# Optimization experiments

Measured on AMD Instinct MI355X. Metric: run time of the kernel, lower is better.

Reference implementation:

```python
import jax, jax.numpy as jnp
import numpy as np

K = 512
DIM = 256
BETA = 0.25


def setup_inputs() -> dict:
    key = jax.random.key(0)
    k1, k2 = jax.random.split(key)
    x = jax.random.normal(k1, (64, DIM, 32, 32), dtype=jnp.float32)
    lookup_table = jax.random.normal(k2, (K, DIM), dtype=jnp.float32)
    return {"x": x, "lookup_table": lookup_table}


def reference(x, lookup_table):
    b, d, h, w = x.shape
    # [b,d,h,w] -> [b*h*w, d]
    xf = jnp.transpose(x, (0, 2, 3, 1)).reshape(-1, d)
    # Squared Euclidean distances (argmin identical to torch.cdist argmin)
    d2 = (
        jnp.sum(xf * xf, axis=-1, keepdims=True)
        - 2.0 * (xf @ lookup_table.T)
        + jnp.sum(lookup_table * lookup_table, axis=-1)
    )  # [N, K]
    q = jnp.argmin(d2, axis=1)  # [N]
    x_e = lookup_table[q].reshape(b, h, w, d).transpose(0, 3, 1, 2)  # [b,d,h,w]
    q_x = q.reshape(b, h, w)
    codebook_loss = jnp.mean(jnp.square(jax.lax.stop_gradient(x) - x_e))
    commitment_loss = jnp.mean(jnp.square(x - jax.lax.stop_gradient(x_e)))
    loss = codebook_loss + BETA * commitment_loss
    return x_e, q_x, loss
```

## Files before the change

### kernel.cpp

```cpp
#include <hip/hip_runtime.h>

#define DIM     256
#define HW      1024
#define N_ROWS  65536
#define NT      256
#define QBM     32
#define NBLK    2048
#define MARGIN  0.25f
#define MARGIN3 0.375f

#define OUT_Q_OFF    16777216
#define OUT_LOSS_OFF 16842752

#define WS_DIST    512
#define WS_X2      2560
#define WS_LUTH_B  786432

#define VQ_LDS 49152

typedef _Float16 half8v __attribute__((ext_vector_type(8)));
typedef float floatx4 __attribute__((ext_vector_type(4)));

#define GLOAD_LDS16(gaddr, laddr) \
    __builtin_amdgcn_global_load_lds((const __attribute__((address_space(1))) unsigned int*)(gaddr), \
                                     (__attribute__((address_space(3))) unsigned int*)(laddr), 16, 0, 0)

__global__ void c2_kernel(const float* __restrict__ lut, float* __restrict__ ws) {
    int t = threadIdx.x;
    for (int k = t; k < 512; k += 256) {
        const float4* row = (const float4*)(lut + (size_t)k * DIM);
        float s = 0.f;
        #pragma unroll 8
        for (int i = 0; i < DIM / 4; ++i) {
            float4 v = row[i];
            s += v.x * v.x + v.y * v.y + v.z * v.z + v.w * v.w;
        }
        ws[k] = s;
    }
}

__global__ void lutprep_kernel(const float* __restrict__ lut, float* __restrict__ ws) {
    int g = blockIdx.x * 256 + threadIdx.x;
    int lane = g & 63;
    int ctu  = (g >> 6) & 31;
    int dcg  = g >> 11;
    int code = ctu * 16 + (lane & 15);
    int d0   = dcg * 32 + (lane >> 4) * 8;
    const float* src = lut + (size_t)code * DIM + d0;
    half8v h;
    #pragma unroll
    for (int j = 0; j < 8; ++j) h[j] = (_Float16)src[j];
    char* dst = (char*)ws + WS_LUTH_B + (size_t)(dcg * 32 + ctu) * 1024 + lane * 16;
    *(half8v*)dst = h;
}

#define MERGE_TRIPLE(v1,i1,v2,i2,v3, w1,j1,w2,j2,w3)                          \
    {                                                                         \
        float a1,a2,a3,b1v,b2v; int a1i,a2i,b1i,b2i;                          \
        bool bf = (w1 < v1) || (w1 == v1 && j1 < i1);                         \
        if (bf) { a1=w1;a1i=j1;a2=w2;a2i=j2;a3=w3; b1v=v1;b1i=i1;b2v=v2;b2i=i2; } \
        else    { a1=v1;a1i=i1;a2=v2;a2i=i2;a3=v3; b1v=w1;b1i=j1;b2v=w2;b2i=j2; } \
        bool sa = (a2 < b1v) || (a2 == b1v && a2i < b1i);                     \
        v1 = a1; i1 = a1i;                                                    \
        if (sa) { v2 = a2; i2 = a2i; v3 = fminf(a3, b1v); }                   \
        else    { v2 = b1v; i2 = b1i; v3 = fminf(a2, b2v); }                  \
    }

__global__ __launch_bounds__(NT, 3) void vq_kernel(const float* __restrict__ x,
                                                   const float* __restrict__ lut,
                                                   float* __restrict__ out,
                                                   float* __restrict__ ws) {
    extern __shared__ char smem[];
    char* asmem = smem + 32768;
    const char* luth = (const char*)ws + WS_LUTH_B;

    const int tid = threadIdx.x;
    const int blk = blockIdx.x;
    const int n0  = blk * QBM;
    const int b   = n0 >> 10;
    const int hw0 = n0 & 1023;
    const float* xb = x + (size_t)b * (DIM * HW) + hw0;

    const int wave = tid >> 6;
    const int lane = tid & 63;
    const int l15  = lane & 15;
    const int l4   = lane >> 4;
    const int cg   = wave;

    float x2local = 0.f;
    {
        const int h = tid & 7;
        const int g = tid >> 3;
        const int dc = g >> 2, o = g & 3;
        float4 v[8];
        #pragma unroll
        for (int j = 0; j < 8; ++j)
            v[j] = *(const float4*)(xb + (size_t)(8 * g + j) * HW + 4 * h);
        #pragma unroll
        for (int j = 0; j < 8; ++j) {
            x2local = fmaf(v[j].x, v[j].x, x2local);
            x2local = fmaf(v[j].y, v[j].y, x2local);
            x2local = fmaf(v[j].z, v[j].z, x2local);
            x2local = fmaf(v[j].w, v[j].w, x2local);
        }
        #pragma unroll
        for (int r = 0; r < 4; ++r) {
            int row = 4 * h + r;
            half8v hh;
            #pragma unroll
            for (int j = 0; j < 8; ++j) {
                const float* vf = (const float*)&v[j];
                hh[j] = (_Float16)vf[r];
            }
            char* dst = asmem + (size_t)((row >> 4) * 8 + dc) * 1024 + (((row & 15) + 16 * o) * 16);
            *(half8v*)dst = hh;
        }
    }

    floatx4 acc[2][8];
    #pragma unroll
    for (int i = 0; i < 2; ++i)
        #pragma unroll
        for (int j = 0; j < 8; ++j) acc[i][j] = (floatx4)0.f;

    #pragma unroll
    for (int i = 0; i < 8; ++i) {
        int cc = wave * 8 + i;
        GLOAD_LDS16(luth + (size_t)(0 * 32 + cc) * 1024 + lane * 16, smem + cc * 1024);
    }
    __syncthreads();

    for (int dc = 0; dc < 8; ++dc) {
        asm volatile("s_waitcnt vmcnt(0)" ::: "memory");
        __builtin_amdgcn_sched_barrier(0);
        half8v ah[2], bh[8];
        #pragma unroll
        for (int rtl = 0; rtl < 2; ++rtl)
            ah[rtl] = *(const half8v*)(asmem + (size_t)(rtl * 8 + dc) * 1024 + lane * 16);
        #pragma unroll
        for (int ct = 0; ct < 8; ++ct)
            bh[ct] = *(const half8v*)(smem + (size_t)(cg * 8 + ct) * 1024 + lane * 16);
        asm volatile("s_waitcnt lgkmcnt(0)" ::: "memory");
        __builtin_amdgcn_sched_barrier(0);
        if (dc < 7) {
            #pragma unroll
            for (int i = 0; i < 8; ++i) {
                int cc = wave * 8 + i;
                GLOAD_LDS16(luth + (size_t)((dc + 1) * 32 + cc) * 1024 + lane * 16, smem + cc * 1024);
            }
        }
        #pragma unroll
        for (int ct = 0; ct < 8; ++ct)
            #pragma unroll
            for (int rtl = 0; rtl < 2; ++rtl)
                acc[rtl][ct] = __builtin_amdgcn_mfma_f32_16x16x32_f16(ah[rtl], bh[ct], acc[rtl][ct], 0, 0, 0);
    }
    __syncthreads();

    float* rv1   = (float*)smem;
    int*   ri1   = (int*)(smem + 512);
    float* rv2   = (float*)(smem + 1024);
    int*   ri2   = (int*)(smem + 1536);
    float* rv3   = (float*)(smem + 2048);
    int*   qsh   = (int*)(smem + 2560);
    float* wsumx = (float*)(smem + 2688);
    int*   fl_cnt = (int*)(smem + 2704);
    int*   fl_row = (int*)(smem + 2720);
    int*   fl_ia  = (int*)(smem + 2848);
    int*   fl_ib  = (int*)(smem + 2976);
    int*   fl_md  = (int*)(smem + 3104);
    float* xrow  = (float*)(smem + 3328);
    float* carow = (float*)(smem + 4352);
    float* cbrow = (float*)(smem + 5376);
    float* frv   = (float*)(smem + 6400);
    int*   fri   = (int*)(smem + 7424);

    if (tid == 0) *fl_cnt = 0;

    #pragma unroll
    for (int rt = 0; rt < 2; ++rt) {
        #pragma unroll
        for (int r = 0; r < 4; ++r) {
            float v1 = 3.4e38f, v2 = 3.4e38f, v3 = 3.4e38f; int i1 = 0, i2 = 0;
            #pragma unroll
            for (int ct = 0; ct < 8; ++ct) {
                int code = (cg * 8 + ct) * 16 + l15;
                float dist = fmaf(-2.f, acc[rt][ct][r], ws[code]);
                if (dist < v1)      { v3 = v2; v2 = v1; i2 = i1; v1 = dist; i1 = code; }
                else if (dist < v2) { v3 = v2; v2 = dist; i2 = code; }
                else if (dist < v3) { v3 = dist; }
            }
            #pragma unroll
            for (int off = 1; off < 16; off <<= 1) {
                float w1 = __shfl_xor(v1, off, 64);
                int   j1 = __shfl_xor(i1, off, 64);
                float w2 = __shfl_xor(v2, off, 64);
                int   j2 = __shfl_xor(i2, off, 64);
                float w3 = __shfl_xor(v3, off, 64);
                MERGE_TRIPLE(v1, i1, v2, i2, v3, w1, j1, w2, j2, w3);
            }
            if (l15 == 0) {
                int idx = cg * 32 + rt * 16 + l4 * 4 + r;
                rv1[idx] = v1; ri1[idx] = i1; rv2[idx] = v2; ri2[idx] = i2; rv3[idx] = v3;
            }
        }
    }
    __syncthreads();

    float dist_part = 0.f;
    if (tid < QBM) {
        const int row = tid;
        float m1 = rv1[row]; int n1 = ri1[row]; float m2 = rv2[row]; int n2 = ri2[row]; float m3 = rv3[row];
        #pragma unroll
        for (int s = 1; s < 4; ++s) {
            float w1 = rv1[s * 32 + row]; int j1 = ri1[s * 32 + row];
            float w2 = rv2[s * 32 + row]; int j2 = ri2[s * 32 + row];
            float w3 = rv3[s * 32 + row];
            MERGE_TRIPLE(m1, n1, m2, n2, m3, w1, j1, w2, j2, w3);
        }
        qsh[row] = n1;
        if (m2 - m1 <= MARGIN) {
            int idx = atomicAdd(fl_cnt, 1);
            fl_row[idx] = row;
            fl_ia[idx]  = n1;
            fl_ib[idx]  = n2;
            fl_md[idx]  = (m3 - m1 <= MARGIN3) ? 1 : 0;
        }
        dist_part = m1;
    }
    float dv = dist_part;
    #pragma unroll
    for (int off = 32; off; off >>= 1) dv += __shfl_down(dv, off, 64);
    if (tid == 0) ws[WS_DIST + blk] = dv;
    float xv = x2local;
    #pragma unroll
    for (int off = 32; off; off >>= 1) xv += __shfl_down(xv, off, 64);
    if (lane == 0) wsumx[wave] = xv;
    __syncthreads();
    if (tid == 0) ws[WS_X2 + blk] = wsumx[0] + wsumx[1] + wsumx[2] + wsumx[3];

    const int nfl = *fl_cnt;
    for (int ii = 0; ii < nfl; ++ii) {
        const int row = fl_row[ii];
        const int ia  = fl_ia[ii];
        const int ib  = fl_ib[ii];
        const int md  = fl_md[ii];
        xrow[tid]  = xb[(size_t)tid * HW + row];
        carow[tid] = lut[(size_t)ia * DIM + tid];
        cbrow[tid] = lut[(size_t)ib * DIM + tid];
        __syncthreads();
        if (md == 0) {
            if (tid == 0) {
                float dota = 0.f, dotb = 0.f;
                for (int d = 0; d < DIM; ++d) {
                    dota = fmaf(xrow[d], carow[d], dota);
                    dotb = fmaf(xrow[d], cbrow[d], dotb);
                }
                float da = fmaf(-2.f, dota, ws[ia]);
                float db = fmaf(-2.f, dotb, ws[ib]);
                int q;
                if (da < db) q = ia;
                else if (db < da) q = ib;
                else q = (ia < ib) ? ia : ib;
                qsh[row] = q;
            }
        } else {
            float bv = 3.4e38f; int bi = 0;
            #pragma unroll
            for (int k2 = 0; k2 < 2; ++k2) {
                int k = tid + k2 * 256;
                const float* cr = lut + (size_t)k * DIM;
                float dot = 0.f;
                for (int d = 0; d < DIM; ++d) dot = fmaf(xrow[d], cr[d], dot);
                float dist = fmaf(-2.f, dot, ws[k]);
                if (dist < bv || (dist == bv && k < bi)) { bv = dist; bi = k; }
            }
            frv[tid] = bv; fri[tid] = bi;
            __syncthreads();
            for (int s = 128; s; s >>= 1) {
                if (tid < s) {
                    float ov = frv[tid + s]; int oi = fri[tid + s];
                    if (ov < frv[tid] || (ov == frv[tid] && oi < fri[tid])) {
                        frv[tid] = ov; fri[tid] = oi;
                    }
                }
                __syncthreads();
            }
            if (tid == 0) qsh[row] = fri[0];
        }
        __syncthreads();
    }

    if (tid < QBM) out[OUT_Q_OFF + n0 + tid] = (float)qsh[tid];

    {
        const int h = tid & 7;
        const int g = tid >> 3;
        int qs[4];
        #pragma unroll
        for (int r = 0; r < 4; ++r) qs[r] = qsh[4 * h + r];
        float* ob = out + (size_t)b * (DIM * HW) + hw0 + 4 * h;
        #pragma unroll
        for (int j = 0; j < 8; ++j) {
            int d = 8 * g + j;
            float4 c;
            float* cp = (float*)&c;
            #pragma unroll
            for (int r = 0; r < 4; ++r) cp[r] = lut[(size_t)qs[r] * DIM + d];
            *(float4*)(ob + (size_t)d * HW) = c;
        }
    }
}

__global__ void loss_kernel(float* __restrict__ out, const float* __restrict__ ws) {
    __shared__ float wsum[4];
    int tid = threadIdx.x;
    float s = 0.f;
    for (int i = tid; i < 4096; i += 256) s += ws[WS_DIST + i];
    #pragma unroll
    for (int off = 32; off; off >>= 1) s += __shfl_down(s, off, 64);
    if ((tid & 63) == 0) wsum[tid >> 6] = s;
    __syncthreads();
    if (tid == 0) {
        float total = wsum[0] + wsum[1] + wsum[2] + wsum[3];
        out[OUT_LOSS_OFF] = total * (1.25f / 16777216.f);
    }
}

extern "C" void kernel_launch(void* const* d_in, const int* in_sizes, int n_in,
                              void* d_out, int out_size, void* d_ws, size_t ws_size,
                              hipStream_t stream) {
    const float* x   = (const float*)d_in[0];
    const float* lut = (const float*)d_in[1];
    float* out = (float*)d_out;
    float* ws  = (float*)d_ws;

    (void)hipFuncSetAttribute((const void*)vq_kernel,
                              hipFuncAttributeMaxDynamicSharedMemorySize, VQ_LDS);

    c2_kernel<<<1, 256, 0, stream>>>(lut, ws);
    lutprep_kernel<<<64, 256, 0, stream>>>(lut, ws);
    vq_kernel<<<NBLK, NT, VQ_LDS, stream>>>(x, lut, out, ws);
    loss_kernel<<<1, 256, 0, stream>>>(out, ws);
}
```

Measured before the change: 130.5 us.

## Move ambiguous-row fp32 rechecks into a separate global worklist kernel

The in-block serial recheck loop for rows whose fp16 top-two distances are close is removed from the main VQ kernel. Candidate rows are now appended to global worklists via atomics, and a new recheck kernel spread across many blocks recomputes them in fp32 and overwrites the index and quantized output. The tie margins are also halved, so fewer rows get rechecked. This removes load imbalance and stalls in the main kernel, at the cost of an extra launch, global atomics, and a higher risk of wrong argmins from the tighter margin; the loss still uses the fp16 min distances.

```diff
diff --git a/kernel.cpp b/kernel.cpp
--- a/kernel.cpp
+++ b/kernel.cpp
@@ -6,14 +6,20 @@
 #define NT      256
 #define QBM     32
 #define NBLK    2048
-#define MARGIN  0.25f
-#define MARGIN3 0.375f
+#define MARGIN  0.125f
+#define MARGIN3 0.1875f
 
 #define OUT_Q_OFF    16777216
 #define OUT_LOSS_OFF 16842752
 
 #define WS_DIST    512
 #define WS_X2      2560
+#define WS_CNTF_I  4608
+#define WS_CNTP_I  4609
+#define WS_LISTF_I 5120
+#define WS_LISTP_I 21504
+#define CAP_F      16384
+#define CAP_P      32768
 #define WS_LUTH_B  786432
 
 #define VQ_LDS 49152
@@ -26,6 +32,7 @@
                                      (__attribute__((address_space(3))) unsigned int*)(laddr), 16, 0, 0)
 
 __global__ void c2_kernel(const float* __restrict__ lut, float* __restrict__ ws) {
+    if (threadIdx.x == 0) { ((int*)ws)[WS_CNTF_I] = 0; ((int*)ws)[WS_CNTP_I] = 0; }
     int t = threadIdx.x;
     for (int k = t; k < 512; k += 256) {
         const float4* row = (const float4*)(lut + (size_t)k * DIM);
@@ -164,18 +171,6 @@
     float* rv3   = (float*)(smem + 2048);
     int*   qsh   = (int*)(smem + 2560);
     float* wsumx = (float*)(smem + 2688);
-    int*   fl_cnt = (int*)(smem + 2704);
-    int*   fl_row = (int*)(smem + 2720);
-    int*   fl_ia  = (int*)(smem + 2848);
-    int*   fl_ib  = (int*)(smem + 2976);
-    int*   fl_md  = (int*)(smem + 3104);
-    float* xrow  = (float*)(smem + 3328);
-    float* carow = (float*)(smem + 4352);
-    float* cbrow = (float*)(smem + 5376);
-    float* frv   = (float*)(smem + 6400);
-    int*   fri   = (int*)(smem + 7424);
-
-    if (tid == 0) *fl_cnt = 0;
 
     #pragma unroll
     for (int rt = 0; rt < 2; ++rt) {
@@ -219,12 +214,19 @@
             MERGE_TRIPLE(m1, n1, m2, n2, m3, w1, j1, w2, j2, w3);
         }
         qsh[row] = n1;
+        out[OUT_Q_OFF + n0 + row] = (float)n1;
         if (m2 - m1 <= MARGIN) {
-            int idx = atomicAdd(fl_cnt, 1);
-            fl_row[idx] = row;
-            fl_ia[idx]  = n1;
-            fl_ib[idx]  = n2;
-            fl_md[idx]  = (m3 - m1 <= MARGIN3) ? 1 : 0;
+            if (m3 - m1 > MARGIN3) {
+                int idx = atomicAdd((int*)ws + WS_CNTP_I, 1);
+                if (idx < CAP_P) {
+                    ((int*)ws)[WS_LISTP_I + idx * 3 + 0] = n0 + row;
+                    ((int*)ws)[WS_LISTP_I + idx * 3 + 1] = n1;
+                    ((int*)ws)[WS_LISTP_I + idx * 3 + 2] = n2;
+                }
+            } else {
+                int idx = atomicAdd((int*)ws + WS_CNTF_I, 1);
+                if (idx < CAP_F) ((int*)ws)[WS_LISTF_I + idx] = n0 + row;
+            }
         }
         dist_part = m1;
     }
@@ -232,66 +234,13 @@
     #pragma unroll
     for (int off = 32; off; off >>= 1) dv += __shfl_down(dv, off, 64);
     if (tid == 0) ws[WS_DIST + blk] = dv;
+
     float xv = x2local;
     #pragma unroll
     for (int off = 32; off; off >>= 1) xv += __shfl_down(xv, off, 64);
     if (lane == 0) wsumx[wave] = xv;
     __syncthreads();
     if (tid == 0) ws[WS_X2 + blk] = wsumx[0] + wsumx[1] + wsumx[2] + wsumx[3];
-
-    const int nfl = *fl_cnt;
-    for (int ii = 0; ii < nfl; ++ii) {
-        const int row = fl_row[ii];
-        const int ia  = fl_ia[ii];
-        const int ib  = fl_ib[ii];
-        const int md  = fl_md[ii];
-        xrow[tid]  = xb[(size_t)tid * HW + row];
-        carow[tid] = lut[(size_t)ia * DIM + tid];
-        cbrow[tid] = lut[(size_t)ib * DIM + tid];
-        __syncthreads();
-        if (md == 0) {
-            if (tid == 0) {
-                float dota = 0.f, dotb = 0.f;
-                for (int d = 0; d < DIM; ++d) {
-                    dota = fmaf(xrow[d], carow[d], dota);
-                    dotb = fmaf(xrow[d], cbrow[d], dotb);
-                }
-                float da = fmaf(-2.f, dota, ws[ia]);
-                float db = fmaf(-2.f, dotb, ws[ib]);
-                int q;
-                if (da < db) q = ia;
-                else if (db < da) q = ib;
-                else q = (ia < ib) ? ia : ib;
-                qsh[row] = q;
-            }
-        } else {
-            float bv = 3.4e38f; int bi = 0;
-            #pragma unroll
-            for (int k2 = 0; k2 < 2; ++k2) {
-                int k = tid + k2 * 256;
-                const float* cr = lut + (size_t)k * DIM;
-                float dot = 0.f;
-                for (int d = 0; d < DIM; ++d) dot = fmaf(xrow[d], cr[d], dot);
-                float dist = fmaf(-2.f, dot, ws[k]);
-                if (dist < bv || (dist == bv && k < bi)) { bv = dist; bi = k; }
-            }
-            frv[tid] = bv; fri[tid] = bi;
-            __syncthreads();
-            for (int s = 128; s; s >>= 1) {
-                if (tid < s) {
-                    float ov = frv[tid + s]; int oi = fri[tid + s];
-                    if (ov < frv[tid] || (ov == frv[tid] && oi < fri[tid])) {
-                        frv[tid] = ov; fri[tid] = oi;
-                    }
-                }
-                __syncthreads();
-            }
-            if (tid == 0) qsh[row] = fri[0];
-        }
-        __syncthreads();
-    }
-
-    if (tid < QBM) out[OUT_Q_OFF + n0 + tid] = (float)qsh[tid];
 
     {
         const int h = tid & 7;
@@ -309,6 +258,85 @@
             for (int r = 0; r < 4; ++r) cp[r] = lut[(size_t)qs[r] * DIM + d];
             *(float4*)(ob + (size_t)d * HW) = c;
         }
+    }
+}
+
+__global__ void recheck_kernel(const float* __restrict__ x, const float* __restrict__ lut,
+                               float* __restrict__ out, const float* __restrict__ ws) {
+    __shared__ float xrow[DIM];
+    __shared__ float carow[DIM];
+    __shared__ float cbrow[DIM];
+    __shared__ float frv[256];
+    __shared__ int   fri[256];
+    __shared__ int   qq;
+    const int tid = threadIdx.x;
+
+    int cntp = ((const int*)ws)[WS_CNTP_I];
+    if (cntp > CAP_P) cntp = CAP_P;
+    const int* lp = (const int*)ws + WS_LISTP_I;
+    for (int e = blockIdx.x; e < cntp; e += gridDim.x) {
+        const int row = lp[e * 3 + 0];
+        const int ia  = lp[e * 3 + 1];
+        const int ib  = lp[e * 3 + 2];
+        const int b = row >> 10, hw = row & 1023;
+        xrow[tid]  = x[(size_t)b * (DIM * HW) + (size_t)tid * HW + hw];
+        carow[tid] = lut[(size_t)ia * DIM + tid];
+        cbrow[tid] = lut[(size_t)ib * DIM + tid];
+        __syncthreads();
+        if (tid == 0) {
+            float dota = 0.f, dotb = 0.f;
+            for (int d = 0; d < DIM; ++d) {
+                dota = fmaf(xrow[d], carow[d], dota);
+                dotb = fmaf(xrow[d], cbrow[d], dotb);
+            }
+            float da = fmaf(-2.f, dota, ws[ia]);
+            float db = fmaf(-2.f, dotb, ws[ib]);
+            int q;
+            if (da < db) q = ia;
+            else if (db < da) q = ib;
+            else q = (ia < ib) ? ia : ib;
+            qq = q;
+            out[OUT_Q_OFF + row] = (float)q;
+        }
+        __syncthreads();
+        const int q = qq;
+        out[(size_t)b * (DIM * HW) + (size_t)tid * HW + hw] = lut[(size_t)q * DIM + tid];
+        __syncthreads();
+    }
+
+    int cntf = ((const int*)ws)[WS_CNTF_I];
+    if (cntf > CAP_F) cntf = CAP_F;
+    const int* lf = (const int*)ws + WS_LISTF_I;
+    for (int e = blockIdx.x; e < cntf; e += gridDim.x) {
+        const int row = lf[e];
+        const int b = row >> 10, hw = row & 1023;
+        xrow[tid] = x[(size_t)b * (DIM * HW) + (size_t)tid * HW + hw];
+        __syncthreads();
+        float bv = 3.4e38f; int bi = 0;
+        #pragma unroll
+        for (int k2 = 0; k2 < 2; ++k2) {
+            int k = tid + k2 * 256;
+            const float* cr = lut + (size_t)k * DIM;
+            float dot = 0.f;
+            for (int d = 0; d < DIM; ++d) dot = fmaf(xrow[d], cr[d], dot);
+            float dist = fmaf(-2.f, dot, ws[k]);
+            if (dist < bv || (dist == bv && k < bi)) { bv = dist; bi = k; }
+        }
+        frv[tid] = bv; fri[tid] = bi;
+        __syncthreads();
+        for (int s = 128; s; s >>= 1) {
+            if (tid < s) {
+                float ov = frv[tid + s]; int oi = fri[tid + s];
+                if (ov < frv[tid] || (ov == frv[tid] && oi < fri[tid])) {
+                    frv[tid] = ov; fri[tid] = oi;
+                }
+            }
+            __syncthreads();
+        }
+        const int q = fri[0];
+        if (tid == 0) out[OUT_Q_OFF + row] = (float)q;
+        out[(size_t)b * (DIM * HW) + (size_t)tid * HW + hw] = lut[(size_t)q * DIM + tid];
+        __syncthreads();
     }
 }
 
@@ -341,5 +369,6 @@
     c2_kernel<<<1, 256, 0, stream>>>(lut, ws);
     lutprep_kernel<<<64, 256, 0, stream>>>(lut, ws);
     vq_kernel<<<NBLK, NT, VQ_LDS, stream>>>(x, lut, out, ws);
+    recheck_kernel<<<2048, 256, 0, stream>>>(x, lut, out, ws);
     loss_kernel<<<1, 256, 0, stream>>>(out, ws);
 }
```

Result: faster. 126.3 us (-3.2%).
